# Performance work log

Hardware: AMD Instinct MI355X
Metric: run time of the kernel (lower is better)

## Reference

```python
import jax, jax.numpy as jnp
import numpy as np

NUM_HEADS = 4
GROUPS = 8
EPS = 1e-5


def setup_inputs() -> dict:
    key = jax.random.key(0)
    k1, k2, k3 = jax.random.split(key, 3)
    B, C, H, W = 2, 256, 64, 64
    x = jax.random.normal(k1, (B, C, H, W), dtype=jnp.float32)
    gn_gamma = jnp.ones((C,), dtype=jnp.float32)
    gn_beta = jnp.zeros((C,), dtype=jnp.float32)
    w_qkv = jax.random.normal(k2, (3 * C, C), dtype=jnp.float32) * (C ** -0.5)
    w_proj = jax.random.normal(k3, (C, C), dtype=jnp.float32) * (C ** -0.5)
    b_proj = jnp.zeros((C,), dtype=jnp.float32)
    return {"x": x, "gn_gamma": gn_gamma, "gn_beta": gn_beta,
            "w_qkv": w_qkv, "w_proj": w_proj, "b_proj": b_proj}


def group_norm(x, gamma, beta):
    B, C, H, W = x.shape
    xg = x.reshape(B, GROUPS, C // GROUPS, H, W)
    mean = xg.mean(axis=(2, 3, 4), keepdims=True)
    var = xg.var(axis=(2, 3, 4), keepdims=True)  # biased, matching torch GroupNorm
    xn = ((xg - mean) * jax.lax.rsqrt(var + EPS)).reshape(B, C, H, W)
    return xn * gamma[None, :, None, None] + beta[None, :, None, None]


def reference(x, gn_gamma, gn_beta, w_qkv, w_proj, b_proj):
    B, C, H, W = x.shape
    nh = NUM_HEADS
    d = C // nh
    xn = group_norm(x, gn_gamma, gn_beta)  # note: residual uses normalized x, as in source
    # 1x1 conv == channel matmul: [B,3C,H,W] -> [B,3,nh,d,HW]
    qkv = jnp.einsum('bchw,oc->bohw', xn, w_qkv).reshape(B, 3, nh, d, H * W)
    q, k, v = qkv[:, 0], qkv[:, 1], qkv[:, 2]  # each [B, nh, d, HW]
    scores = jnp.einsum('bhci,bhcj->bhij', q, k) * (d ** -0.5)  # [B, nh, HW, HW]
    attn = jax.nn.softmax(scores, axis=-1)
    out = jnp.einsum('bhij,bhcj->bhci', attn, v).reshape(B, C, H, W)
    proj = jnp.einsum('bchw,oc->bohw', out, w_proj) + b_proj[None, :, None, None]
    return xn + proj
```

## Files before the change

kernel.cpp:

```cpp
#include <hip/hip_runtime.h>


typedef short s16x8 __attribute__((ext_vector_type(8)));
typedef float f32x4 __attribute__((ext_vector_type(4)));

#define MFMA16(a, b, c) __builtin_amdgcn_mfma_f32_16x16x32_bf16(a, b, c, 0, 0, 0)

__device__ __forceinline__ short bf16s(float f) {
  union { float f; unsigned u; } v; v.f = f;
  unsigned r = v.u + 0x7fffu + ((v.u >> 16) & 1u);
  return (short)(r >> 16);
}

__device__ __forceinline__ unsigned cvtpk(float lo, float hi) {
  unsigned r;
  asm("v_cvt_pk_bf16_f32 %0, %1, %2" : "=v"(r) : "v"(lo), "v"(hi));
  return r;
}

__device__ __forceinline__ float exp_raw(float x) {
  return __builtin_amdgcn_exp2f(x);
}

__device__ __forceinline__ void gload16(const void* g, void* l) {
  __builtin_amdgcn_global_load_lds(
      (const __attribute__((address_space(1))) unsigned*)g,
      (__attribute__((address_space(3))) unsigned*)l, 16, 0, 0);
}

__global__ __launch_bounds__(256) void prep_w(const float* __restrict__ wq,
                                              const float* __restrict__ wp,
                                              short* __restrict__ wqb,
                                              short* __restrict__ wpb) {
  int i = blockIdx.x * 256 + threadIdx.x;
  if (i < 768 * 256) {
    wqb[i] = bf16s(wq[i]);
  } else {
    int j = i - 768 * 256;
    if (j < 256 * 256) wpb[j] = bf16s(wp[j]);
  }
}

__global__ __launch_bounds__(256) void gn_partial(const float* __restrict__ x,
                                                  float* __restrict__ part) {
  int blk = blockIdx.x;
  int gi = blk >> 4, sub = blk & 15;
  const float* base = x + (long)gi * 131072 + sub * 8192;
  int t = threadIdx.x;
  float s = 0.f, ss = 0.f;
#pragma unroll
  for (int k = 0; k < 8; k++) {
    float4 v = *(const float4*)(base + t * 4 + k * 1024);
    s += v.x + v.y + v.z + v.w;
    ss += v.x * v.x + v.y * v.y + v.z * v.z + v.w * v.w;
  }
#pragma unroll
  for (int m = 1; m < 64; m <<= 1) { s += __shfl_xor(s, m); ss += __shfl_xor(ss, m); }
  __shared__ float red[8];
  int wv = t >> 6;
  if ((t & 63) == 0) { red[wv * 2] = s; red[wv * 2 + 1] = ss; }
  __syncthreads();
  if (t == 0) {
    float S = 0.f, SS = 0.f;
    for (int w = 0; w < 4; w++) { S += red[w * 2]; SS += red[w * 2 + 1]; }
    part[blk * 2] = S; part[blk * 2 + 1] = SS;
  }
}

__device__ __forceinline__ void stats_prologue(const float* __restrict__ part,
                                               float* sstats, int t) {
  if (t < 16) {
    float S = 0.f, SS = 0.f;
#pragma unroll
    for (int i = 0; i < 16; i++) {
      S += part[(t * 16 + i) * 2];
      SS += part[(t * 16 + i) * 2 + 1];
    }
    float mean = S * (1.0f / 131072.0f);
    float var = SS * (1.0f / 131072.0f) - mean * mean;
    sstats[t * 2] = mean;
    sstats[t * 2 + 1] = rsqrtf(var + 1e-5f);
  }
}

__global__ __launch_bounds__(256) void gn_norm_t(const float* __restrict__ x,
                                                 const float* __restrict__ gamma,
                                                 const float* __restrict__ beta,
                                                 const float* __restrict__ part,
                                                 short* __restrict__ xnT) {
  __shared__ __align__(16) short T[64 * 88];
  __shared__ float sstats[32];
  int bx = blockIdx.x;
  int pt = bx & 63, ct = (bx >> 6) & 3, b = bx >> 8;
  int t = threadIdx.x;
  stats_prologue(part, sstats, t);
  __syncthreads();
#pragma unroll
  for (int it = 0; it < 4; it++) {
    int chunk = t + it * 256;
    int c_loc = chunk >> 4, pch = chunk & 15;
    int c = ct * 64 + c_loc;
    int g = b * 8 + (c >> 5);
    float mean = sstats[g * 2], rstd = sstats[g * 2 + 1];
    float ga = gamma[c] * rstd;
    float be = beta[c] - mean * ga;
    long idx = ((long)(b * 256 + c)) * 4096 + pt * 64 + pch * 4;
    float4 v = *(const float4*)(x + idx);
    float4 n = {v.x * ga + be, v.y * ga + be, v.z * ga + be, v.w * ga + be};
    int p0 = pch * 4;
    T[(p0 + 0) * 88 + c_loc] = bf16s(n.x);
    T[(p0 + 1) * 88 + c_loc] = bf16s(n.y);
    T[(p0 + 2) * 88 + c_loc] = bf16s(n.z);
    T[(p0 + 3) * 88 + c_loc] = bf16s(n.w);
  }
  __syncthreads();
#pragma unroll
  for (int it = 0; it < 2; it++) {
    int chunk = t + it * 256;
    int p_loc = chunk >> 3, cch = chunk & 7;
    s16x8 v = *(const s16x8*)&T[p_loc * 88 + cch * 8];
    *(s16x8*)&xnT[((long)(b * 4096 + pt * 64 + p_loc)) * 256 + ct * 64 + cch * 8] = v;
  }
}

__global__ __launch_bounds__(256) void qkv_gemm(const short* __restrict__ xnT,
                                                const short* __restrict__ wqb,
                                                short* __restrict__ qT,
                                                short* __restrict__ kP,
                                                short* __restrict__ vP) {
  __shared__ __align__(16) short As[128 * 32];
  __shared__ __align__(16) short Bs[128 * 32];
  int m0 = blockIdx.x * 128, n0 = blockIdx.y * 128, b = blockIdx.z;
  const short* A = xnT + (long)b * 4096 * 256;
  int t = threadIdx.x, wv = t >> 6, lane = t & 63, lg = lane >> 4, lq = lane & 15;
  int wr = wv >> 1, wc = wv & 1;
  f32x4 acc[4][4] = {};
  for (int kt = 0; kt < 8; kt++) {
    int k0 = kt * 32;
#pragma unroll
    for (int it = 0; it < 2; it++) {
      int chunk = t + it * 256;
      int row = chunk >> 2, kch = chunk & 3;
      int kk = kch ^ ((row >> 1) & 3);
      gload16(A + (m0 + row) * 256 + k0 + kk * 8, &As[it * 2048 + wv * 512]);
      gload16(wqb + (n0 + row) * 256 + k0 + kk * 8, &Bs[it * 2048 + wv * 512]);
    }
    __syncthreads();
    s16x8 af[4], bfr[4];
#pragma unroll
    for (int mi = 0; mi < 4; mi++) {
      int row = wr * 64 + mi * 16 + lq;
      af[mi] = *(const s16x8*)&As[row * 32 + ((lg ^ ((row >> 1) & 3)) << 3)];
    }
#pragma unroll
    for (int ni = 0; ni < 4; ni++) {
      int row = wc * 64 + ni * 16 + lq;
      bfr[ni] = *(const s16x8*)&Bs[row * 32 + ((lg ^ ((row >> 1) & 3)) << 3)];
    }
#pragma unroll
    for (int mi = 0; mi < 4; mi++)
#pragma unroll
      for (int ni = 0; ni < 4; ni++)
        acc[mi][ni] = MFMA16(af[mi], bfr[ni], acc[mi][ni]);
    __syncthreads();
  }
  if (blockIdx.y < 2) {
    short* Out = qT + (long)b * 4096 * 256;
#pragma unroll
    for (int mi = 0; mi < 4; mi++)
#pragma unroll
      for (int ni = 0; ni < 4; ni++) {
        int p = m0 + wr * 64 + mi * 16 + (lg << 2);
        int o = n0 + wc * 64 + ni * 16 + lq;
#pragma unroll
        for (int r = 0; r < 4; r++)
          Out[(long)(p + r) * 256 + o] = bf16s(acc[mi][ni][r] * 0.180336880f);
      }
  } else if (blockIdx.y < 4) {
#pragma unroll
    for (int mi = 0; mi < 4; mi++)
#pragma unroll
      for (int ni = 0; ni < 4; ni++) {
        int p = m0 + wr * 64 + mi * 16 + (lg << 2);
        int kcol = (n0 - 256) + wc * 64 + ni * 16 + lq;
        int h = kcol >> 6, ch = kcol & 63;
        int fc = (ch & 32) ? 1 : 0;
        int lgp = (ch & 31) >> 3, e = ch & 7;
        long base = ((long)(b * 4 + h)) * 128 * 2048;
#pragma unroll
        for (int r = 0; r < 4; r++) {
          int j = p + r;
          int tile = j >> 5, r32 = j & 31;
          int fr = (r32 & 4) ? 2 : 0;
          int lqp = (r32 & 3) + 4 * (r32 >> 3);
          kP[base + (long)tile * 2048 + (fr + fc) * 512 + (lgp * 16 + lqp) * 8 + e] =
              bf16s(acc[mi][ni][r]);
        }
      }
  } else {
#pragma unroll
    for (int mi = 0; mi < 4; mi++)
#pragma unroll
      for (int ni = 0; ni < 4; ni++) {
        int p = m0 + wr * 64 + mi * 16 + (lg << 2);
        int c = (n0 - 512) + wc * 64 + ni * 16 + lq;
        int h = c >> 6, ch = c & 63;
        int f = ch >> 4, lqp = ch & 15;
        int tile = p >> 5, lgp = (p & 31) >> 3, e0 = p & 7;
        unsigned u0 = cvtpk(acc[mi][ni][0], acc[mi][ni][1]);
        unsigned u1 = cvtpk(acc[mi][ni][2], acc[mi][ni][3]);
        *(unsigned long long*)&vP[((long)(b * 4 + h) * 128 + tile) * 2048 +
                                  f * 512 + (lgp * 16 + lqp) * 8 + e0] =
            ((unsigned long long)u1 << 32) | u0;
      }
  }
}

#define LOADKV(KF, VF, JT)                                                  \
  do {                                                                      \
    long tb_ = ((long)((JT) * 4 + wv)) * 2048 + l * 8;                      \
    KF##0 = *(const s16x8*)(kp + tb_);                                      \
    KF##1 = *(const s16x8*)(kp + tb_ + 512);                                \
    KF##2 = *(const s16x8*)(kp + tb_ + 1024);                               \
    KF##3 = *(const s16x8*)(kp + tb_ + 1536);                               \
    VF##0 = *(const s16x8*)(vp + tb_);                                      \
    VF##1 = *(const s16x8*)(vp + tb_ + 512);                                \
    VF##2 = *(const s16x8*)(vp + tb_ + 1024);                               \
    VF##3 = *(const s16x8*)(vp + tb_ + 1536);                               \
  } while (0)

#define COMPUTE(KF, VF)                                                     \
  do {                                                                      \
    _Pragma("unroll") for (int ig = 0; ig < 4; ig++) {                      \
      f32x4 z0 = {0.f, 0.f, 0.f, 0.f}, z1 = {0.f, 0.f, 0.f, 0.f};           \
      z0 = MFMA16(KF##0, qf[ig][0], z0);                                    \
      z0 = MFMA16(KF##1, qf[ig][1], z0);                                    \
      z1 = MFMA16(KF##2, qf[ig][0], z1);                                    \
      z1 = MFMA16(KF##3, qf[ig][1], z1);                                    \
      f32x4 p0, p1;                                                         \
      _Pragma("unroll") for (int r = 0; r < 4; r++) {                       \
        p0[r] = exp_raw(z0[r]);                                             \
        p1[r] = exp_raw(z1[r]);                                             \
      }                                                                     \
      f32x4 ps = p0 + p1;                                                   \
      lsc[ig] += (ps[0] + ps[1]) + (ps[2] + ps[3]);                         \
      union { unsigned u[4]; s16x8 v; } pb;                                 \
      pb.u[0] = cvtpk(p0[0], p0[1]);                                        \
      pb.u[1] = cvtpk(p0[2], p0[3]);                                        \
      pb.u[2] = cvtpk(p1[0], p1[1]);                                        \
      pb.u[3] = cvtpk(p1[2], p1[3]);                                        \
      oacc[ig][0] = MFMA16(VF##0, pb.v, oacc[ig][0]);                       \
      oacc[ig][1] = MFMA16(VF##1, pb.v, oacc[ig][1]);                       \
      oacc[ig][2] = MFMA16(VF##2, pb.v, oacc[ig][2]);                       \
      oacc[ig][3] = MFMA16(VF##3, pb.v, oacc[ig][3]);                       \
    }                                                                       \
  } while (0)

__global__ __launch_bounds__(256, 2) void attn(const short* __restrict__ qT_,
                                               const short* __restrict__ kP,
                                               const short* __restrict__ vP,
                                               short* __restrict__ ao_) {
  __shared__ __align__(16) f32x4 cb[2 * 1088];
  int bid = blockIdx.x;
  int bh = bid & 7, itile = bid >> 3;
  int b = bh >> 2, h = bh & 3;
  int i0 = itile * 64;
  const short* kp = kP + (long)bh * 128 * 2048;
  const short* vp = vP + (long)bh * 128 * 2048;
  short* ao = ao_ + (long)b * 4096 * 256;
  int t = threadIdx.x, wv = t >> 6, l = t & 63, lq = l & 15, lg = l >> 4;

  s16x8 qf[4][2];
  const short* qbase = qT_ + (long)b * 4096 * 256 + h * 64;
#pragma unroll
  for (int ig = 0; ig < 4; ig++) {
    const short* qr = qbase + (long)(i0 + ig * 16 + lq) * 256;
    qf[ig][0] = *(const s16x8*)(qr + 8 * lg);
    qf[ig][1] = *(const s16x8*)(qr + 32 + 8 * lg);
  }

  f32x4 oacc[4][4] = {};
  float lsc[4] = {0.f, 0.f, 0.f, 0.f};

  s16x8 ka0, ka1, ka2, ka3, va0, va1, va2, va3;
  s16x8 kb0, kb1, kb2, kb3, vb0, vb1, vb2, vb3;

  LOADKV(ka, va, 0);
  for (int jt = 0; jt < 32; jt += 2) {
    LOADKV(kb, vb, jt + 1);
    COMPUTE(ka, va);
    if (jt + 2 < 32) LOADKV(ka, va, jt + 2);
    COMPUTE(kb, vb);
  }

  f32x4 lv4;
#pragma unroll
  for (int ig = 0; ig < 4; ig++) {
    float s = lsc[ig];
    s += __shfl_xor(s, 16);
    s += __shfl_xor(s, 32);
    lv4[ig] = s;
  }

#define CB_W(REG)                                                           \
  do {                                                                      \
    f32x4* d_ = cb + (REG) * 1088;                                          \
    _Pragma("unroll") for (int ig = 0; ig < 4; ig++)                        \
    _Pragma("unroll") for (int nc = 0; nc < 4; nc++)                        \
        d_[(ig * 4 + nc) * 64 + l] = oacc[ig][nc];                          \
    d_[16 * 64 + l] = lv4;                                                  \
  } while (0)
#define CB_A(REG)                                                           \
  do {                                                                      \
    f32x4* s_ = cb + (REG) * 1088;                                          \
    _Pragma("unroll") for (int ig = 0; ig < 4; ig++)                        \
    _Pragma("unroll") for (int nc = 0; nc < 4; nc++)                        \
        oacc[ig][nc] += s_[(ig * 4 + nc) * 64 + l];                         \
    lv4 += s_[16 * 64 + l];                                                 \
  } while (0)

  if (wv >= 2) CB_W(wv - 2);
  __syncthreads();
  if (wv < 2) CB_A(wv);
  __syncthreads();
  if (wv == 1) CB_W(0);
  __syncthreads();
  if (wv == 0) {
    CB_A(0);
#pragma unroll
    for (int ig = 0; ig < 4; ig++) {
      float inv = 1.0f / lv4[ig];
      long irow = i0 + ig * 16 + lq;
#pragma unroll
      for (int nc = 0; nc < 4; nc++) {
        f32x4 o = oacc[ig][nc];
        unsigned u0 = cvtpk(o[0] * inv, o[1] * inv);
        unsigned u1 = cvtpk(o[2] * inv, o[3] * inv);
        *(unsigned long long*)&ao[irow * 256 + h * 64 + nc * 16 + 4 * lg] =
            ((unsigned long long)u1 << 32) | u0;
      }
    }
  }
}

__global__ __launch_bounds__(256) void proj_gemm(const short* __restrict__ ao,
                                                 const short* __restrict__ wpb,
                                                 const float* __restrict__ bproj,
                                                 const float* __restrict__ x,
                                                 const float* __restrict__ gamma,
                                                 const float* __restrict__ beta,
                                                 const float* __restrict__ part,
                                                 float* __restrict__ out) {
  __shared__ __align__(16) short As[128 * 32];
  __shared__ __align__(16) short Bs[128 * 32];
  __shared__ float sstats[32];
  int m0 = blockIdx.x * 128, n0 = blockIdx.y * 128, b = blockIdx.z;
  const short* A = ao + (long)b * 4096 * 256;
  int t = threadIdx.x, wv = t >> 6, lane = t & 63, lg = lane >> 4, lq = lane & 15;
  int wr = wv >> 1, wc = wv & 1;
  stats_prologue(part, sstats, t);
  f32x4 acc[4][4] = {};
  for (int kt = 0; kt < 8; kt++) {
    int k0 = kt * 32;
#pragma unroll
    for (int it = 0; it < 2; it++) {
      int chunk = t + it * 256;
      int row = chunk >> 2, kch = chunk & 3;
      int kk = kch ^ ((row >> 1) & 3);
      gload16(A + (m0 + row) * 256 + k0 + kk * 8, &As[it * 2048 + wv * 512]);
      gload16(wpb + (n0 + row) * 256 + k0 + kk * 8, &Bs[it * 2048 + wv * 512]);
    }
    __syncthreads();
    s16x8 af[4], bfr[4];
#pragma unroll
    for (int mi = 0; mi < 4; mi++) {
      int row = wr * 64 + mi * 16 + lq;
      af[mi] = *(const s16x8*)&As[row * 32 + ((lg ^ ((row >> 1) & 3)) << 3)];
    }
#pragma unroll
    for (int ni = 0; ni < 4; ni++) {
      int row = wc * 64 + ni * 16 + lq;
      bfr[ni] = *(const s16x8*)&Bs[row * 32 + ((lg ^ ((row >> 1) & 3)) << 3)];
    }
#pragma unroll
    for (int mi = 0; mi < 4; mi++)
#pragma unroll
      for (int ni = 0; ni < 4; ni++)
        acc[mi][ni] = MFMA16(af[mi], bfr[ni], acc[mi][ni]);
    __syncthreads();
  }
#pragma unroll
  for (int mi = 0; mi < 4; mi++)
#pragma unroll
    for (int ni = 0; ni < 4; ni++) {
      int p = m0 + wr * 64 + mi * 16 + (lg << 2);
      int o = n0 + wc * 64 + ni * 16 + lq;
      int g = b * 8 + (o >> 5);
      float mean = sstats[g * 2], rstd = sstats[g * 2 + 1];
      float ga = gamma[o] * rstd;
      float be = beta[o] - mean * ga + bproj[o];
      long idx = ((long)(b * 256 + o)) * 4096 + p;
      float4 xv = *(const float4*)(x + idx);
      float4 ov = {acc[mi][ni][0] + xv.x * ga + be, acc[mi][ni][1] + xv.y * ga + be,
                   acc[mi][ni][2] + xv.z * ga + be, acc[mi][ni][3] + xv.w * ga + be};
      *(float4*)(out + idx) = ov;
    }
}

extern "C" void kernel_launch(void* const* d_in, const int* in_sizes, int n_in,
                              void* d_out, int out_size, void* d_ws, size_t ws_size,
                              hipStream_t stream) {
  const float* x = (const float*)d_in[0];
  const float* gamma = (const float*)d_in[1];
  const float* beta = (const float*)d_in[2];
  const float* wq = (const float*)d_in[3];
  const float* wp = (const float*)d_in[4];
  const float* bp = (const float*)d_in[5];
  float* out = (float*)d_out;
  char* ws = (char*)d_ws;

  short* xnT = (short*)(ws + 0);
  short* wqb = (short*)(ws + 4194304);
  short* wpb = (short*)(ws + 4587520);
  short* qT = (short*)(ws + 4718592);
  short* kP = (short*)(ws + 8912896);
  short* vP = (short*)(ws + 13107200);
  short* ao = (short*)(ws + 17301504);
  float* gpart = (float*)(ws + 21495808);

  prep_w<<<1024, 256, 0, stream>>>(wq, wp, wqb, wpb);
  gn_partial<<<256, 256, 0, stream>>>(x, gpart);
  gn_norm_t<<<512, 256, 0, stream>>>(x, gamma, beta, gpart, xnT);
  qkv_gemm<<<dim3(32, 6, 2), 256, 0, stream>>>(xnT, wqb, qT, kP, vP);
  attn<<<512, 256, 0, stream>>>(qT, kP, vP, ao);
  proj_gemm<<<dim3(32, 2, 2), 256, 0, stream>>>(ao, wpb, bp, x, gamma, beta, gpart, out);
}
```

Measured before the change: 76.27 us.

## Merge weight prep into GN stats kernel, halve GEMM M-tiles, stage K stores via LDS

Folds the weight bf16 conversion kernel into the group-norm partial-stats kernel, removing one launch. Halves the M tile of both the QKV and projection GEMMs from 128 to 64 rows, doubling the block count from 384 to 768 and from 128 to 256 to fill more CUs, at the cost of less reuse of each weight tile. K-output stores now go through an LDS transpose so each thread writes 16-byte vectors instead of scattered 2-byte stores.

```diff
diff --git a/kernel.cpp b/kernel.cpp
--- a/kernel.cpp
+++ b/kernel.cpp
@@ -28,25 +28,26 @@
       (__attribute__((address_space(3))) unsigned*)l, 16, 0, 0);
 }
 
-__global__ __launch_bounds__(256) void prep_w(const float* __restrict__ wq,
+__global__ __launch_bounds__(256) void pre_gn(const float* __restrict__ x,
+                                              const float* __restrict__ wq,
                                               const float* __restrict__ wp,
                                               short* __restrict__ wqb,
-                                              short* __restrict__ wpb) {
-  int i = blockIdx.x * 256 + threadIdx.x;
-  if (i < 768 * 256) {
-    wqb[i] = bf16s(wq[i]);
-  } else {
-    int j = i - 768 * 256;
-    if (j < 256 * 256) wpb[j] = bf16s(wp[j]);
-  }
-}
-
-__global__ __launch_bounds__(256) void gn_partial(const float* __restrict__ x,
-                                                  float* __restrict__ part) {
+                                              short* __restrict__ wpb,
+                                              float* __restrict__ part) {
   int blk = blockIdx.x;
+  int t = threadIdx.x;
+  if (blk >= 256) {
+    int i = (blk - 256) * 256 + t;
+    if (i < 768 * 256) {
+      wqb[i] = bf16s(wq[i]);
+    } else {
+      int j = i - 768 * 256;
+      if (j < 256 * 256) wpb[j] = bf16s(wp[j]);
+    }
+    return;
+  }
   int gi = blk >> 4, sub = blk & 15;
   const float* base = x + (long)gi * 131072 + sub * 8192;
-  int t = threadIdx.x;
   float s = 0.f, ss = 0.f;
 #pragma unroll
   for (int k = 0; k < 8; k++) {
@@ -128,28 +129,33 @@
                                                 short* __restrict__ qT,
                                                 short* __restrict__ kP,
                                                 short* __restrict__ vP) {
-  __shared__ __align__(16) short As[128 * 32];
-  __shared__ __align__(16) short Bs[128 * 32];
-  int m0 = blockIdx.x * 128, n0 = blockIdx.y * 128, b = blockIdx.z;
+  __shared__ __align__(16) short smem[8320];
+  short* As = smem;
+  short* Bs = smem + 2048;
+  int m0 = blockIdx.x * 64, n0 = blockIdx.y * 128, b = blockIdx.z;
   const short* A = xnT + (long)b * 4096 * 256;
   int t = threadIdx.x, wv = t >> 6, lane = t & 63, lg = lane >> 4, lq = lane & 15;
   int wr = wv >> 1, wc = wv & 1;
-  f32x4 acc[4][4] = {};
+  f32x4 acc[2][4] = {};
   for (int kt = 0; kt < 8; kt++) {
     int k0 = kt * 32;
+    {
+      int row = t >> 2, kch = t & 3;
+      int kk = kch ^ ((row >> 1) & 3);
+      gload16(A + (m0 + row) * 256 + k0 + kk * 8, &As[wv * 512]);
+    }
 #pragma unroll
     for (int it = 0; it < 2; it++) {
       int chunk = t + it * 256;
       int row = chunk >> 2, kch = chunk & 3;
       int kk = kch ^ ((row >> 1) & 3);
-      gload16(A + (m0 + row) * 256 + k0 + kk * 8, &As[it * 2048 + wv * 512]);
       gload16(wqb + (n0 + row) * 256 + k0 + kk * 8, &Bs[it * 2048 + wv * 512]);
     }
     __syncthreads();
-    s16x8 af[4], bfr[4];
-#pragma unroll
-    for (int mi = 0; mi < 4; mi++) {
-      int row = wr * 64 + mi * 16 + lq;
+    s16x8 af[2], bfr[4];
+#pragma unroll
+    for (int mi = 0; mi < 2; mi++) {
+      int row = wr * 32 + mi * 16 + lq;
       af[mi] = *(const s16x8*)&As[row * 32 + ((lg ^ ((row >> 1) & 3)) << 3)];
     }
 #pragma unroll
@@ -158,7 +164,7 @@
       bfr[ni] = *(const s16x8*)&Bs[row * 32 + ((lg ^ ((row >> 1) & 3)) << 3)];
     }
 #pragma unroll
-    for (int mi = 0; mi < 4; mi++)
+    for (int mi = 0; mi < 2; mi++)
 #pragma unroll
       for (int ni = 0; ni < 4; ni++)
         acc[mi][ni] = MFMA16(af[mi], bfr[ni], acc[mi][ni]);
@@ -167,42 +173,45 @@
   if (blockIdx.y < 2) {
     short* Out = qT + (long)b * 4096 * 256;
 #pragma unroll
-    for (int mi = 0; mi < 4; mi++)
+    for (int mi = 0; mi < 2; mi++)
 #pragma unroll
       for (int ni = 0; ni < 4; ni++) {
-        int p = m0 + wr * 64 + mi * 16 + (lg << 2);
+        int p = m0 + wr * 32 + mi * 16 + (lg << 2);
         int o = n0 + wc * 64 + ni * 16 + lq;
 #pragma unroll
         for (int r = 0; r < 4; r++)
           Out[(long)(p + r) * 256 + o] = bf16s(acc[mi][ni][r] * 0.180336880f);
       }
   } else if (blockIdx.y < 4) {
-#pragma unroll
-    for (int mi = 0; mi < 4; mi++)
+    short(*Ts)[130] = (short(*)[130])smem;
+#pragma unroll
+    for (int mi = 0; mi < 2; mi++)
 #pragma unroll
       for (int ni = 0; ni < 4; ni++) {
-        int p = m0 + wr * 64 + mi * 16 + (lg << 2);
-        int kcol = (n0 - 256) + wc * 64 + ni * 16 + lq;
-        int h = kcol >> 6, ch = kcol & 63;
-        int fc = (ch & 32) ? 1 : 0;
-        int lgp = (ch & 31) >> 3, e = ch & 7;
-        long base = ((long)(b * 4 + h)) * 128 * 2048;
-#pragma unroll
-        for (int r = 0; r < 4; r++) {
-          int j = p + r;
-          int tile = j >> 5, r32 = j & 31;
-          int fr = (r32 & 4) ? 2 : 0;
-          int lqp = (r32 & 3) + 4 * (r32 >> 3);
-          kP[base + (long)tile * 2048 + (fr + fc) * 512 + (lgp * 16 + lqp) * 8 + e] =
-              bf16s(acc[mi][ni][r]);
-        }
+        int pr = wr * 32 + mi * 16 + (lg << 2);
+        int oc = wc * 64 + ni * 16 + lq;
+#pragma unroll
+        for (int r = 0; r < 4; r++) Ts[pr + r][oc] = bf16s(acc[mi][ni][r]);
       }
+    __syncthreads();
+    int reg = t >> 6;
+    int tl = reg >> 1, hl = reg & 1;
+    int l2 = t & 63, lq2 = l2 & 15, lg2 = l2 >> 4;
+    int hb = (n0 - 256) >> 6;
+    long kb2 = ((long)(b * 4 + hb + hl) * 128 + (m0 >> 5) + tl) * 2048;
+#pragma unroll
+    for (int f = 0; f < 4; f++) {
+      int row = 32 * tl + (lq2 & 3) + 8 * (lq2 >> 2) + 4 * (f >> 1);
+      int col = hl * 64 + 32 * (f & 1) + 8 * lg2;
+      s16x8 v = *(const s16x8*)&Ts[row][col];
+      *(s16x8*)&kP[kb2 + f * 512 + l2 * 8] = v;
+    }
   } else {
 #pragma unroll
-    for (int mi = 0; mi < 4; mi++)
+    for (int mi = 0; mi < 2; mi++)
 #pragma unroll
       for (int ni = 0; ni < 4; ni++) {
-        int p = m0 + wr * 64 + mi * 16 + (lg << 2);
+        int p = m0 + wr * 32 + mi * 16 + (lg << 2);
         int c = (n0 - 512) + wc * 64 + ni * 16 + lq;
         int h = c >> 6, ch = c & 63;
         int f = ch >> 4, lqp = ch & 15;
@@ -351,30 +360,34 @@
                                                  const float* __restrict__ beta,
                                                  const float* __restrict__ part,
                                                  float* __restrict__ out) {
-  __shared__ __align__(16) short As[128 * 32];
+  __shared__ __align__(16) short As[64 * 32];
   __shared__ __align__(16) short Bs[128 * 32];
   __shared__ float sstats[32];
-  int m0 = blockIdx.x * 128, n0 = blockIdx.y * 128, b = blockIdx.z;
+  int m0 = blockIdx.x * 64, n0 = blockIdx.y * 128, b = blockIdx.z;
   const short* A = ao + (long)b * 4096 * 256;
   int t = threadIdx.x, wv = t >> 6, lane = t & 63, lg = lane >> 4, lq = lane & 15;
   int wr = wv >> 1, wc = wv & 1;
   stats_prologue(part, sstats, t);
-  f32x4 acc[4][4] = {};
+  f32x4 acc[2][4] = {};
   for (int kt = 0; kt < 8; kt++) {
     int k0 = kt * 32;
+    {
+      int row = t >> 2, kch = t & 3;
+      int kk = kch ^ ((row >> 1) & 3);
+      gload16(A + (m0 + row) * 256 + k0 + kk * 8, &As[wv * 512]);
+    }
 #pragma unroll
     for (int it = 0; it < 2; it++) {
       int chunk = t + it * 256;
       int row = chunk >> 2, kch = chunk & 3;
       int kk = kch ^ ((row >> 1) & 3);
-      gload16(A + (m0 + row) * 256 + k0 + kk * 8, &As[it * 2048 + wv * 512]);
       gload16(wpb + (n0 + row) * 256 + k0 + kk * 8, &Bs[it * 2048 + wv * 512]);
     }
     __syncthreads();
-    s16x8 af[4], bfr[4];
-#pragma unroll
-    for (int mi = 0; mi < 4; mi++) {
-      int row = wr * 64 + mi * 16 + lq;
+    s16x8 af[2], bfr[4];
+#pragma unroll
+    for (int mi = 0; mi < 2; mi++) {
+      int row = wr * 32 + mi * 16 + lq;
       af[mi] = *(const s16x8*)&As[row * 32 + ((lg ^ ((row >> 1) & 3)) << 3)];
     }
 #pragma unroll
@@ -383,17 +396,17 @@
       bfr[ni] = *(const s16x8*)&Bs[row * 32 + ((lg ^ ((row >> 1) & 3)) << 3)];
     }
 #pragma unroll
-    for (int mi = 0; mi < 4; mi++)
+    for (int mi = 0; mi < 2; mi++)
 #pragma unroll
       for (int ni = 0; ni < 4; ni++)
         acc[mi][ni] = MFMA16(af[mi], bfr[ni], acc[mi][ni]);
     __syncthreads();
   }
 #pragma unroll
-  for (int mi = 0; mi < 4; mi++)
+  for (int mi = 0; mi < 2; mi++)
 #pragma unroll
     for (int ni = 0; ni < 4; ni++) {
-      int p = m0 + wr * 64 + mi * 16 + (lg << 2);
+      int p = m0 + wr * 32 + mi * 16 + (lg << 2);
       int o = n0 + wc * 64 + ni * 16 + lq;
       int g = b * 8 + (o >> 5);
       float mean = sstats[g * 2], rstd = sstats[g * 2 + 1];
@@ -428,10 +441,9 @@
   short* ao = (short*)(ws + 17301504);
   float* gpart = (float*)(ws + 21495808);
 
-  prep_w<<<1024, 256, 0, stream>>>(wq, wp, wqb, wpb);
-  gn_partial<<<256, 256, 0, stream>>>(x, gpart);
+  pre_gn<<<1280, 256, 0, stream>>>(x, wq, wp, wqb, wpb, gpart);
   gn_norm_t<<<512, 256, 0, stream>>>(x, gamma, beta, gpart, xnT);
-  qkv_gemm<<<dim3(32, 6, 2), 256, 0, stream>>>(xnT, wqb, qT, kP, vP);
+  qkv_gemm<<<dim3(64, 6, 2), 256, 0, stream>>>(xnT, wqb, qT, kP, vP);
   attn<<<512, 256, 0, stream>>>(qT, kP, vP, ao);
-  proj_gemm<<<dim3(32, 2, 2), 256, 0, stream>>>(ao, wpb, bp, x, gamma, beta, gpart, out);
-}
+  proj_gemm<<<dim3(64, 2, 2), 256, 0, stream>>>(ao, wpb, bp, x, gamma, beta, gpart, out);
+}
```

Result: faster. 69.17 us (-9.3%).
